# Kernel optimization log

Hardware: AMD Instinct MI355X
Metric: run time of the kernel (lower is better)

Reference implementation:

```python
import jax, jax.numpy as jnp
import numpy as np

B, S, H = 1, 2048, 1024
NH, NKV, HD = 16, 4, 64
I, E, K = 2816, 8, 2
WIN = 512
EPS = 1e-5


def setup_inputs() -> dict:
    key = jax.random.key(0)
    ks = jax.random.split(key, 8)
    sd = 0.02
    return {
        "hidden_states": jax.random.normal(ks[0], (B, S, H), jnp.float32),
        "positions": jnp.arange(S, dtype=jnp.int64),
        "w_qkv": jax.random.normal(ks[1], ((NH + 2 * NKV) * HD, H), jnp.float32) * sd,
        "w_o": jax.random.normal(ks[2], (H, NH * HD), jnp.float32) * sd,
        "router_w": jax.random.normal(ks[3], (E, H), jnp.float32) * sd,
        "ws": jax.random.normal(ks[4], (E, 2 * I, H), jnp.float32) * sd,
        "w2s": jax.random.normal(ks[5], (E, H, I), jnp.float32) * sd,
        "ln1_w": jnp.ones((H,), jnp.float32),
        "ln2_w": jnp.ones((H,), jnp.float32),
    }


def _rmsnorm(x, w):
    return x * jax.lax.rsqrt(jnp.mean(x * x, axis=-1, keepdims=True) + EPS) * w


def reference(hidden_states, positions, w_qkv, w_o, router_w, ws, w2s, ln1_w, ln2_w):
    # residual is None on entry -> residual = input, then input_layernorm
    residual = hidden_states
    x = _rmsnorm(hidden_states, ln1_w)

    # qkv projection (torch Linear: y = x @ W.T), GQA split
    qkv = jnp.einsum("bsh,oh->bso", x, w_qkv)
    q_size, kv_size = NH * HD, NKV * HD
    q = qkv[..., :q_size].reshape(B, S, NH, HD)
    k = qkv[..., q_size:q_size + kv_size].reshape(B, S, NKV, HD)
    v = qkv[..., q_size + kv_size:].reshape(B, S, NKV, HD)
    rep = NH // NKV
    k = jnp.repeat(k, rep, axis=2)  # [B,S,NH,HD]
    v = jnp.repeat(v, rep, axis=2)

    scale = HD ** -0.5
    scores = jnp.einsum("bqhd,bkhd->bhqk", q, k) * scale
    i = jnp.arange(S)[:, None]
    j = jnp.arange(S)[None, :]
    mask = (j <= i) & ((i - j) < WIN)  # causal sliding window
    scores = jnp.where(mask, scores, jnp.finfo(scores.dtype).min)
    attn = jax.nn.softmax(scores, axis=-1)
    o = jnp.einsum("bhqk,bkhd->bqhd", attn, v).reshape(B, S, NH * HD)
    attn_out = jnp.einsum("bso,ho->bsh", o, w_o)

    # pre_moe_layernorm with residual: x += residual; residual = x; x = norm(x)
    x2 = attn_out + residual
    residual2 = x2
    h = _rmsnorm(x2, ln2_w)

    # MoE: router softmax, top-k (renormalize=False), per-expert SwiGLU FFN
    t = h.reshape(-1, H)  # [T,H]
    logits = jnp.einsum("th,eh->te", t, router_w)
    probs = jax.nn.softmax(logits, axis=-1)
    vals, idx = jax.lax.top_k(probs, K)  # [T,K]
    w_dense = jnp.sum(vals[:, :, None] * jax.nn.one_hot(idx, E, dtype=t.dtype), axis=1)  # [T,E]

    out = jnp.zeros_like(t)
    for e in range(E):
        gu = jnp.einsum("th,ih->ti", t, ws[e])  # [T,2I]
        g, u = gu[:, :I], gu[:, I:]
        a = jax.nn.silu(g) * u
        y = jnp.einsum("ti,hi->th", a, w2s[e])
        out = out + w_dense[:, e:e + 1] * y

    return out.reshape(B, S, H), residual2
```

## Files before the change

### kernel.cpp

```cpp
#include <hip/hip_runtime.h>
#include <stdint.h>

typedef unsigned short u16;
typedef __attribute__((ext_vector_type(8))) short short8;
typedef __attribute__((ext_vector_type(4))) float f32x4;

constexpr int SEQ   = 2048;
constexpr int HID   = 1024;
constexpr int NHEAD = 16;
constexpr int QKVD  = 1536;
constexpr int FFI   = 2816;
constexpr int NEXP  = 8;
constexpr int WINSZ = 512;
#define EPSF 1e-5f

__device__ __forceinline__ u16 f2bf(float f) {
  union { unsigned int i; float f; } v; v.f = f;
  unsigned int i = v.i;
  return (u16)((i + 0x7fffu + ((i >> 16) & 1u)) >> 16);
}

__device__ __forceinline__ ushort4 f2bf4(float4 v) {
  ushort4 o;
  o.x = f2bf(v.x); o.y = f2bf(v.y); o.z = f2bf(v.z); o.w = f2bf(v.w);
  return o;
}

__device__ __forceinline__ void gload_lds16(const void* g, void* l) {
  __builtin_amdgcn_global_load_lds((__attribute__((address_space(1))) void*)g,
                                   (__attribute__((address_space(3))) void*)l,
                                   16, 0, 0);
}

#define MFMA_BF16(a, b, c) __builtin_amdgcn_mfma_f32_16x16x32_bf16(a, b, c, 0, 0, 0)

#define TILE_FENCE                                          \
  asm volatile("s_waitcnt vmcnt(0)" ::: "memory");          \
  __builtin_amdgcn_s_barrier();                             \
  __builtin_amdgcn_sched_barrier(0);

constexpr int CN3 = NEXP * 2 * FFI * HID / 4;
constexpr int CN4 = NEXP * HID * FFI / 4;
constexpr int CN_BIG   = CN3 + CN4;
constexpr int NCONV_BLK = CN_BIG / 1024;
constexpr int NATTN_BLK = (SEQ / 64) * NHEAD;

__global__ __launch_bounds__(256) void k_prep(const float* __restrict__ x,
                                              const float* __restrict__ w,
                                              u16* __restrict__ y) {
  const int bid = blockIdx.x, tid = threadIdx.x;
  const int wid = tid >> 6, lane = tid & 63;
  __shared__ float red[4];
  const float* xr = x + (size_t)bid * HID;
  float4 v = *(const float4*)&xr[tid * 4];
  float ss = v.x * v.x + v.y * v.y + v.z * v.z + v.w * v.w;
#pragma unroll
  for (int m = 1; m < 64; m <<= 1) ss += __shfl_xor(ss, m);
  if (lane == 0) red[wid] = ss;
  __syncthreads();
  ss = red[0] + red[1] + red[2] + red[3];
  float sc = rsqrtf(ss * (1.0f / HID) + EPSF);
  float4 wv = *(const float4*)&w[tid * 4];
  ushort4 o;
  o.x = f2bf(v.x * sc * wv.x);
  o.y = f2bf(v.y * sc * wv.y);
  o.z = f2bf(v.z * sc * wv.z);
  o.w = f2bf(v.w * sc * wv.w);
  *(ushort4*)&y[(size_t)bid * HID + tid * 4] = o;
}

__global__ __launch_bounds__(256, 2) void k_gemm_bt(
    const u16* __restrict__ A, const float* __restrict__ B,
    void* __restrict__ Cout, int N, int K, int KT, int wf32) {
  __shared__ u16 As[128 * 64];
  __shared__ u16 Bs[64 * 72];
  const int tid = threadIdx.x, wid = tid >> 6, lane = tid & 63;
  const int quad = lane >> 4, l16 = lane & 15;
  const int wr = wid >> 1, wc = wid & 1;
  const int m0 = blockIdx.y * 128, n0 = blockIdx.x * 64;
  const int M = gridDim.y * 128;
  const int kbase = blockIdx.z * KT * 64;
  const int sr = lane >> 3, sc = (lane & 7) * 8;
  const int brow = wid * 16 + (lane >> 2);
  const int bk = (lane & 3) * 16;
  f32x4 acc[4][2] = {};
  for (int kt = 0; kt < KT; ++kt) {
    const int k0 = kbase + (kt << 6);
    const float* bp = &B[(size_t)(n0 + brow) * K + k0 + bk];
    float4 bv0 = *(const float4*)&bp[0];
    float4 bv1 = *(const float4*)&bp[4];
    float4 bv2 = *(const float4*)&bp[8];
    float4 bv3 = *(const float4*)&bp[12];
#pragma unroll
    for (int it = 0; it < 4; ++it) {
      int seg = wid * 4 + it;
      int row = seg * 8 + sr;
      gload_lds16(&A[(size_t)(m0 + row) * K + k0 + sc], &As[seg * 512]);
    }
    *(ushort4*)&Bs[brow * 72 + bk + 0]  = f2bf4(bv0);
    *(ushort4*)&Bs[brow * 72 + bk + 4]  = f2bf4(bv1);
    *(ushort4*)&Bs[brow * 72 + bk + 8]  = f2bf4(bv2);
    *(ushort4*)&Bs[brow * 72 + bk + 12] = f2bf4(bv3);
    __syncthreads();
#pragma unroll
    for (int ks = 0; ks < 2; ++ks) {
      short8 af[4], bf[2];
#pragma unroll
      for (int t = 0; t < 4; ++t)
        af[t] = *(const short8*)&As[(64 * wr + 16 * t + l16) * 64 + ks * 32 + quad * 8];
#pragma unroll
      for (int t = 0; t < 2; ++t)
        bf[t] = *(const short8*)&Bs[(32 * wc + 16 * t + l16) * 72 + ks * 32 + quad * 8];
#pragma unroll
      for (int mt = 0; mt < 4; ++mt)
#pragma unroll
        for (int nt = 0; nt < 2; ++nt)
          acc[mt][nt] = MFMA_BF16(af[mt], bf[nt], acc[mt][nt]);
    }
    __syncthreads();
  }
  if (wf32) {
    float* C = (float*)Cout + (size_t)blockIdx.z * M * N;
#pragma unroll
    for (int mt = 0; mt < 4; ++mt)
#pragma unroll
      for (int r = 0; r < 4; ++r) {
        int row = m0 + 64 * wr + 16 * mt + quad * 4 + r;
#pragma unroll
        for (int nt = 0; nt < 2; ++nt) {
          int col = n0 + 32 * wc + 16 * nt + l16;
          C[(size_t)row * N + col] = acc[mt][nt][r];
        }
      }
  } else {
    u16* C = (u16*)Cout;
#pragma unroll
    for (int mt = 0; mt < 4; ++mt)
#pragma unroll
      for (int r = 0; r < 4; ++r) {
        int row = m0 + 64 * wr + 16 * mt + quad * 4 + r;
#pragma unroll
        for (int nt = 0; nt < 2; ++nt) {
          int col = n0 + 32 * wc + 16 * nt + l16;
          C[(size_t)row * N + col] = f2bf(acc[mt][nt][r]);
        }
      }
  }
}

__global__ __launch_bounds__(256, 2) void k_attn_conv(
    const u16* __restrict__ qkv, u16* __restrict__ o,
    const float* __restrict__ ws, const float* __restrict__ w2s,
    u16* __restrict__ dws, u16* __restrict__ dw2) {
  const int bid = blockIdx.x;
  const int tid = threadIdx.x;
  if (bid >= NATTN_BLK) {
    int j = (bid - NATTN_BLK) * 1024 + tid;
#pragma unroll
    for (int t = 0; t < 4; ++t) {
      int i = j + t * 256;
      const float* s; u16* d;
      if (i < CN3) { s = ws; d = dws; } else { i -= CN3; s = w2s; d = dw2; }
      float4 v = ((const float4*)s)[i];
      ushort4 u;
      u.x = f2bf(v.x); u.y = f2bf(v.y); u.z = f2bf(v.z); u.w = f2bf(v.w);
      ((ushort4*)d)[i] = u;
    }
    return;
  }
  const int qb = bid & 31;
  const int h  = bid >> 5;
  const int q0 = qb * 64;
  const int g = h >> 2;
  __shared__ u16 Qs[64 * 72], Ks[64 * 72], Vt[64 * 72], Ps[64 * 72];
  const int wid = tid >> 6, lane = tid & 63;
  const int quad = lane >> 4, l16 = lane & 15;

#pragma unroll
  for (int it = 0; it < 2; ++it) {
    int idx = it * 256 + tid;
    int row = idx >> 3, c8 = (idx & 7) * 8;
    *(short8*)&Qs[row * 72 + c8] =
        *(const short8*)&qkv[(size_t)(q0 + row) * QKVD + h * 64 + c8];
  }

  f32x4 oacc[4] = {};
  float mrun[4], lrun[4];
#pragma unroll
  for (int r = 0; r < 4; ++r) { mrun[r] = -1e30f; lrun[r] = 0.f; }

  const int ktlo = (q0 >= WINSZ) ? ((q0 - WINSZ + 1) >> 6) : 0;
  const int kthi = qb;
  for (int kt = ktlo; kt <= kthi; ++kt) {
#pragma unroll
    for (int it = 0; it < 2; ++it) {
      int idx = it * 256 + tid;
      int row = idx >> 3, c8 = (idx & 7) * 8;
      *(short8*)&Ks[row * 72 + c8] =
          *(const short8*)&qkv[(size_t)(kt * 64 + row) * QKVD + 1024 + g * 64 + c8];
    }
#pragma unroll
    for (int it = 0; it < 8; ++it) {
      int idx = it * 256 + tid;
      int key = idx >> 5;
      int d = (idx & 31) * 2;
      unsigned int u = *(const unsigned int*)&qkv[(size_t)(kt * 64 + key) * QKVD + 1280 + g * 64 + d];
      Vt[d * 72 + key] = (u16)(u & 0xffffu);
      Vt[(d + 1) * 72 + key] = (u16)(u >> 16);
    }
    __syncthreads();

    f32x4 sa[4] = {};
#pragma unroll
    for (int ks = 0; ks < 2; ++ks) {
      short8 af = *(const short8*)&Qs[(16 * wid + l16) * 72 + ks * 32 + quad * 8];
#pragma unroll
      for (int ct = 0; ct < 4; ++ct) {
        short8 bf = *(const short8*)&Ks[(16 * ct + l16) * 72 + ks * 32 + quad * 8];
        sa[ct] = MFMA_BF16(af, bf, sa[ct]);
      }
    }

    float pvv[4][4];
#pragma unroll
    for (int r = 0; r < 4; ++r) {
      int i = q0 + 16 * wid + quad * 4 + r;
      float mx = -1e30f;
#pragma unroll
      for (int ct = 0; ct < 4; ++ct) {
        int j = kt * 64 + 16 * ct + l16;
        float v = sa[ct][r] * 0.125f;
        bool ok = (j <= i) && (i - j < WINSZ);
        v = ok ? v : -1e30f;
        pvv[ct][r] = v;
        mx = fmaxf(mx, v);
      }
#pragma unroll
      for (int m = 1; m < 16; m <<= 1) mx = fmaxf(mx, __shfl_xor(mx, m));
      float mnew = fmaxf(mrun[r], mx);
      float alpha = __expf(mrun[r] - mnew);
      float s = 0.f;
#pragma unroll
      for (int ct = 0; ct < 4; ++ct) {
        float p = (pvv[ct][r] > -1e29f) ? __expf(pvv[ct][r] - mnew) : 0.f;
        pvv[ct][r] = p;
        s += p;
      }
#pragma unroll
      for (int m = 1; m < 16; m <<= 1) s += __shfl_xor(s, m);
      lrun[r] = lrun[r] * alpha + s;
      mrun[r] = mnew;
#pragma unroll
      for (int ct = 0; ct < 4; ++ct) oacc[ct][r] *= alpha;
    }
#pragma unroll
    for (int ct = 0; ct < 4; ++ct)
#pragma unroll
      for (int r = 0; r < 4; ++r)
        Ps[(16 * wid + quad * 4 + r) * 72 + 16 * ct + l16] = f2bf(pvv[ct][r]);
    __syncthreads();

#pragma unroll
    for (int ks = 0; ks < 2; ++ks) {
      short8 af = *(const short8*)&Ps[(16 * wid + l16) * 72 + ks * 32 + quad * 8];
#pragma unroll
      for (int ct = 0; ct < 4; ++ct) {
        short8 bf = *(const short8*)&Vt[(16 * ct + l16) * 72 + ks * 32 + quad * 8];
        oacc[ct] = MFMA_BF16(af, bf, oacc[ct]);
      }
    }
    __syncthreads();
  }

#pragma unroll
  for (int ct = 0; ct < 4; ++ct)
#pragma unroll
    for (int r = 0; r < 4; ++r) {
      int row = q0 + 16 * wid + quad * 4 + r;
      float v = oacc[ct][r] / lrun[r];
      o[(size_t)row * HID + h * 64 + 16 * ct + l16] = f2bf(v);
    }
}

__global__ __launch_bounds__(256) void k_rms2_router(
    const float* __restrict__ o0, const float* __restrict__ o1,
    const float* __restrict__ hs, const float* __restrict__ ln2,
    const float* __restrict__ rw, float* __restrict__ out1,
    u16* __restrict__ T, int* __restrict__ counts,
    int* __restrict__ tok_idx, int* __restrict__ tok_slot,
    float* __restrict__ tok_pw) {
  const int tkn = blockIdx.x, tid = threadIdx.x, wid = tid >> 6, lane = tid & 63;
  const size_t base = (size_t)tkn * HID + tid * 4;
  float4 a = *(const float4*)&o0[base];
  float4 b = *(const float4*)&o1[base];
  float4 h = *(const float4*)&hs[base];
  float4 v;
  v.x = a.x + b.x + h.x; v.y = a.y + b.y + h.y;
  v.z = a.z + b.z + h.z; v.w = a.w + b.w + h.w;
  *(float4*)&out1[base] = v;
  float ss = v.x * v.x + v.y * v.y + v.z * v.z + v.w * v.w;
#pragma unroll
  for (int m = 1; m < 64; m <<= 1) ss += __shfl_xor(ss, m);
  __shared__ float red[4];
  if (lane == 0) red[wid] = ss;
  __syncthreads();
  ss = red[0] + red[1] + red[2] + red[3];
  float sc = rsqrtf(ss * (1.0f / HID) + EPSF);
  float4 lw = *(const float4*)&ln2[tid * 4];
  float t0 = v.x * sc * lw.x;
  float t1 = v.y * sc * lw.y;
  float t2 = v.z * sc * lw.z;
  float t3 = v.w * sc * lw.w;
  ushort4 o;
  o.x = f2bf(t0); o.y = f2bf(t1); o.z = f2bf(t2); o.w = f2bf(t3);
  *(ushort4*)&T[(size_t)tkn * HID + tid * 4] = o;

  float p[8];
#pragma unroll
  for (int e = 0; e < 8; ++e) {
    float4 r = *(const float4*)&rw[e * HID + tid * 4];
    p[e] = t0 * r.x + t1 * r.y + t2 * r.z + t3 * r.w;
  }
#pragma unroll
  for (int e = 0; e < 8; ++e)
#pragma unroll
    for (int m = 1; m < 64; m <<= 1) p[e] += __shfl_xor(p[e], m);
  __shared__ float pr[4][8];
  if (lane == 0)
#pragma unroll
    for (int e = 0; e < 8; ++e) pr[wid][e] = p[e];
  __syncthreads();
  if (tid == 0) {
    float lg[8];
#pragma unroll
    for (int e = 0; e < 8; ++e) lg[e] = pr[0][e] + pr[1][e] + pr[2][e] + pr[3][e];
    float mx = lg[0];
#pragma unroll
    for (int e = 1; e < 8; ++e) mx = fmaxf(mx, lg[e]);
    float ex[8], se = 0.f;
#pragma unroll
    for (int e = 0; e < 8; ++e) { ex[e] = __expf(lg[e] - mx); se += ex[e]; }
    int b0 = 0;
#pragma unroll
    for (int e = 1; e < 8; ++e) if (lg[e] > lg[b0]) b0 = e;
    int b1 = (b0 == 0) ? 1 : 0;
#pragma unroll
    for (int e = 0; e < 8; ++e) if (e != b0 && lg[e] > lg[b1]) b1 = e;
    float inv = 1.0f / se;
    int s0 = atomicAdd(&counts[b0], 1);
    tok_idx[b0 * SEQ + s0] = tkn;
    tok_slot[2 * tkn] = b0 * SEQ + s0;
    tok_pw[2 * tkn] = ex[b0] * inv;
    int s1 = atomicAdd(&counts[b1], 1);
    tok_idx[b1 * SEQ + s1] = tkn;
    tok_slot[2 * tkn + 1] = b1 * SEQ + s1;
    tok_pw[2 * tkn + 1] = ex[b1] * inv;
  }
}

__global__ void k_offsets(const int* __restrict__ counts, int* __restrict__ offs) {
  if (threadIdx.x == 0 && blockIdx.x == 0) {
    int s = 0;
    for (int e = 0; e < NEXP; ++e) { offs[e] = s; s += counts[e]; }
    offs[NEXP] = s;
  }
}

__global__ __launch_bounds__(512, 2) void k_moe_gu(
    const u16* __restrict__ T, const u16* __restrict__ Wgu,
    const int* __restrict__ counts, const int* __restrict__ offs,
    const int* __restrict__ tok_idx, u16* __restrict__ Abuf) {
  const int e = blockIdx.z;
  const int cnt = counts[e];
  const int m0 = blockIdx.y * 256;
  if (m0 >= cnt) return;
  const int n0 = blockIdx.x * 128;
  const u16* We = Wgu + (size_t)e * 2 * FFI * HID;
  const int* ti = tok_idx + e * SEQ;
  const int aoff = offs[e];
  __shared__ u16 As[2][256 * 64], Bg[2][128 * 64], Bu[2][128 * 64];
  const int tid = threadIdx.x, wid = tid >> 6, lane = tid & 63;
  const int quad = lane >> 4, l16 = lane & 15;
  const int wr = wid >> 2, wc = wid & 3;
  const int sr = lane >> 3, sc = (lane & 7) * 8;
  int tokrow[4];
#pragma unroll
  for (int it = 0; it < 4; ++it) {
    int row = (wid * 4 + it) * 8 + sr;
    int ra = m0 + row;
    if (ra > cnt - 1) ra = cnt - 1;
    tokrow[it] = ti[ra];
  }
  f32x4 accg[8][2] = {}, accu[8][2] = {};

#define MSTAGE(buf, k0)                                                              \
  {                                                                                  \
    _Pragma("unroll") for (int it = 0; it < 4; ++it) {                               \
      int seg = wid * 4 + it;                                                        \
      gload_lds16(&T[(size_t)tokrow[it] * HID + (k0) + sc], &As[buf][seg * 512]);    \
    }                                                                                \
    _Pragma("unroll") for (int it = 0; it < 2; ++it) {                               \
      int seg = wid * 2 + it;                                                        \
      int row = seg * 8 + sr;                                                        \
      gload_lds16(&We[(size_t)(n0 + row) * HID + (k0) + sc], &Bg[buf][seg * 512]);   \
      gload_lds16(&We[(size_t)(FFI + n0 + row) * HID + (k0) + sc],                   \
                  &Bu[buf][seg * 512]);                                              \
    }                                                                                \
  }
#define MCOMP(buf)                                                                   \
  {                                                                                  \
    _Pragma("unroll") for (int ks = 0; ks < 2; ++ks) {                               \
      short8 af[8], bg[2], bu[2];                                                    \
      _Pragma("unroll") for (int t = 0; t < 8; ++t)                                  \
        af[t] = *(const short8*)&As[buf][(128 * wr + 16 * t + l16) * 64 + ks * 32 +  \
                                         quad * 8];                                  \
      _Pragma("unroll") for (int t = 0; t < 2; ++t) {                                \
        bg[t] = *(const short8*)&Bg[buf][(32 * wc + 16 * t + l16) * 64 + ks * 32 +   \
                                         quad * 8];                                  \
        bu[t] = *(const short8*)&Bu[buf][(32 * wc + 16 * t + l16) * 64 + ks * 32 +   \
                                         quad * 8];                                  \
      }                                                                              \
      _Pragma("unroll") for (int mt = 0; mt < 8; ++mt)                               \
        _Pragma("unroll") for (int nt = 0; nt < 2; ++nt) {                           \
          accg[mt][nt] = MFMA_BF16(af[mt], bg[nt], accg[mt][nt]);                    \
          accu[mt][nt] = MFMA_BF16(af[mt], bu[nt], accu[mt][nt]);                    \
        }                                                                            \
    }                                                                                \
  }

  MSTAGE(0, 0);
  TILE_FENCE
  int cur = 0;
  for (int kt = 0; kt < 16; ++kt) {
    if (kt + 1 < 16) MSTAGE(cur ^ 1, (kt + 1) << 6);
    MCOMP(cur);
    if (kt + 1 < 16) { TILE_FENCE }
    cur ^= 1;
  }
#undef MSTAGE
#undef MCOMP
#pragma unroll
  for (int mt = 0; mt < 8; ++mt)
#pragma unroll
    for (int r = 0; r < 4; ++r) {
      int rl = 128 * wr + 16 * mt + quad * 4 + r;
      int grow = m0 + rl;
      if (grow < cnt) {
        size_t rbase = (size_t)(aoff + grow) * FFI;
#pragma unroll
        for (int nt = 0; nt < 2; ++nt) {
          int col = n0 + 32 * wc + 16 * nt + l16;
          float gv = accg[mt][nt][r];
          float uv = accu[mt][nt][r];
          float a = gv / (1.0f + __expf(-gv)) * uv;
          Abuf[rbase + col] = f2bf(a);
        }
      }
    }
}

__global__ __launch_bounds__(512, 2) void k_moe_y(
    const u16* __restrict__ Abuf, const u16* __restrict__ W2,
    const int* __restrict__ counts, const int* __restrict__ offs,
    float* __restrict__ ybuf) {
  const int e = blockIdx.z >> 1;
  const int sk = blockIdx.z & 1;
  const int cnt = counts[e];
  const int m0 = blockIdx.y * 128;
  if (m0 >= cnt) return;
  const int n0 = blockIdx.x * 256;
  const int kbase = sk * 1408;
  const u16* We = W2 + (size_t)e * HID * FFI;
  const int aoff = offs[e];
  __shared__ u16 As[2][128 * 64], Bs[2][256 * 64];
  const int tid = threadIdx.x, wid = tid >> 6, lane = tid & 63;
  const int quad = lane >> 4, l16 = lane & 15;
  const int wr = wid >> 2, wc = wid & 3;
  const int sr = lane >> 3, sc = (lane & 7) * 8;
  int arow[2];
#pragma unroll
  for (int it = 0; it < 2; ++it) {
    int row = (wid * 2 + it) * 8 + sr;
    int ra = m0 + row;
    if (ra > cnt - 1) ra = cnt - 1;
    arow[it] = aoff + ra;
  }
  f32x4 acc[4][4] = {};

#define YSTAGE(buf, k0)                                                              \
  {                                                                                  \
    _Pragma("unroll") for (int it = 0; it < 2; ++it) {                               \
      int seg = wid * 2 + it;                                                        \
      gload_lds16(&Abuf[(size_t)arow[it] * FFI + (k0) + sc], &As[buf][seg * 512]);   \
    }                                                                                \
    _Pragma("unroll") for (int it = 0; it < 4; ++it) {                               \
      int seg = wid * 4 + it;                                                        \
      int row = seg * 8 + sr;                                                        \
      gload_lds16(&We[(size_t)(n0 + row) * FFI + (k0) + sc], &Bs[buf][seg * 512]);   \
    }                                                                                \
  }
#define YCOMP(buf)                                                                   \
  {                                                                                  \
    _Pragma("unroll") for (int ks = 0; ks < 2; ++ks) {                               \
      short8 af[4], bf[4];                                                           \
      _Pragma("unroll") for (int t = 0; t < 4; ++t)                                  \
        af[t] = *(const short8*)&As[buf][(64 * wr + 16 * t + l16) * 64 + ks * 32 +   \
                                         quad * 8];                                  \
      _Pragma("unroll") for (int t = 0; t < 4; ++t)                                  \
        bf[t] = *(const short8*)&Bs[buf][(64 * wc + 16 * t + l16) * 64 + ks * 32 +   \
                                         quad * 8];                                  \
      _Pragma("unroll") for (int mt = 0; mt < 4; ++mt)                               \
        _Pragma("unroll") for (int nt = 0; nt < 4; ++nt)                             \
            acc[mt][nt] = MFMA_BF16(af[mt], bf[nt], acc[mt][nt]);                    \
    }                                                                                \
  }

  YSTAGE(0, kbase);
  TILE_FENCE
  int cur = 0;
  for (int kt = 0; kt < 22; ++kt) {
    if (kt + 1 < 22) YSTAGE(cur ^ 1, kbase + ((kt + 1) << 6));
    YCOMP(cur);
    if (kt + 1 < 22) { TILE_FENCE }
    cur ^= 1;
  }
#undef YSTAGE
#undef YCOMP
  float* Y = ybuf + (size_t)sk * 2 * SEQ * HID;
#pragma unroll
  for (int mt = 0; mt < 4; ++mt)
#pragma unroll
    for (int r = 0; r < 4; ++r) {
      int rl = 64 * wr + 16 * mt + quad * 4 + r;
      int grow = m0 + rl;
      if (grow < cnt) {
        size_t obase = (size_t)(aoff + grow) * HID;
#pragma unroll
        for (int nt = 0; nt < 4; ++nt) {
          int col = n0 + 64 * wc + 16 * nt + l16;
          Y[obase + col] = acc[mt][nt][r];
        }
      }
    }
}

__global__ __launch_bounds__(256) void k_moe_out(
    const float* __restrict__ yb, const int* __restrict__ offs,
    const int* __restrict__ tok_slot, const float* __restrict__ tok_pw,
    float* __restrict__ out0) {
  const int t = blockIdx.x, tid = threadIdx.x;
  const int v0 = tok_slot[2 * t], v1 = tok_slot[2 * t + 1];
  const float w0 = tok_pw[2 * t], w1 = tok_pw[2 * t + 1];
  const size_t g0 = (size_t)(offs[v0 >> 11] + (v0 & (SEQ - 1))) * HID;
  const size_t g1 = (size_t)(offs[v1 >> 11] + (v1 & (SEQ - 1))) * HID;
  const size_t YP = (size_t)2 * SEQ * HID;
  const int c = tid * 4;
  float4 a0 = *(const float4*)&yb[g0 + c];
  float4 b0 = *(const float4*)&yb[YP + g0 + c];
  float4 a1 = *(const float4*)&yb[g1 + c];
  float4 b1 = *(const float4*)&yb[YP + g1 + c];
  float4 r;
  r.x = w0 * (a0.x + b0.x) + w1 * (a1.x + b1.x);
  r.y = w0 * (a0.y + b0.y) + w1 * (a1.y + b1.y);
  r.z = w0 * (a0.z + b0.z) + w1 * (a1.z + b1.z);
  r.w = w0 * (a0.w + b0.w) + w1 * (a1.w + b1.w);
  *(float4*)&out0[(size_t)t * HID + c] = r;
}

extern "C" void kernel_launch(void* const* d_in, const int* in_sizes, int n_in,
                              void* d_out, int out_size, void* d_ws, size_t ws_size,
                              hipStream_t stream) {
  const float* hs   = (const float*)d_in[0];
  const float* wqkv = (const float*)d_in[2];
  const float* wo   = (const float*)d_in[3];
  const float* rwt  = (const float*)d_in[4];
  const float* wsx  = (const float*)d_in[5];
  const float* w2s  = (const float*)d_in[6];
  const float* ln1  = (const float*)d_in[7];
  const float* ln2  = (const float*)d_in[8];
  float* out0 = (float*)d_out;
  float* out1 = out0 + (size_t)SEQ * HID;

  char* p = (char*)d_ws;
  u16* xn       = (u16*)p;   p += (size_t)SEQ * HID * 2;
  u16* qkv      = (u16*)p;   p += (size_t)SEQ * QKVD * 2;
  u16* ob       = (u16*)p;   p += (size_t)SEQ * HID * 2;
  float* of     = (float*)p; p += (size_t)2 * SEQ * HID * 4;
  int* counts   = (int*)p;   p += 32;
  int* offs     = (int*)p;   p += 64;
  int* tok_idx  = (int*)p;   p += (size_t)NEXP * SEQ * 4;
  int* tok_slot = (int*)p;   p += (size_t)2 * SEQ * 4;
  float* tok_pw = (float*)p; p += (size_t)2 * SEQ * 4;
  u16* abuf     = (u16*)p;   p += (size_t)2 * SEQ * FFI * 2;
  float* ybuf   = (float*)p; p += (size_t)2 * 2 * SEQ * HID * 4;
  u16* ws_b     = (u16*)p;   p += (size_t)NEXP * 2 * FFI * HID * 2;
  u16* w2s_b    = (u16*)p;   p += (size_t)NEXP * HID * FFI * 2;

  u16* tb = xn;

  hipMemsetAsync(counts, 0, 32, stream);

  k_prep<<<SEQ, 256, 0, stream>>>(hs, ln1, xn);
  k_gemm_bt<<<dim3(QKVD / 64, SEQ / 128, 1), 256, 0, stream>>>(
      xn, wqkv, qkv, QKVD, HID, 16, 0);
  k_attn_conv<<<NATTN_BLK + NCONV_BLK, 256, 0, stream>>>(
      qkv, ob, wsx, w2s, ws_b, w2s_b);
  k_gemm_bt<<<dim3(HID / 64, SEQ / 128, 2), 256, 0, stream>>>(
      ob, wo, of, HID, HID, 8, 1);
  k_rms2_router<<<SEQ, 256, 0, stream>>>(of, of + (size_t)SEQ * HID, hs, ln2,
                                         rwt, out1, tb, counts, tok_idx,
                                         tok_slot, tok_pw);
  k_offsets<<<1, 64, 0, stream>>>(counts, offs);
  k_moe_gu<<<dim3(FFI / 128, SEQ / 256, NEXP), 512, 0, stream>>>(
      tb, ws_b, counts, offs, tok_idx, abuf);
  k_moe_y<<<dim3(HID / 256, SEQ / 128, NEXP * 2), 512, 0, stream>>>(
      abuf, w2s_b, counts, offs, ybuf);
  k_moe_out<<<SEQ, 256, 0, stream>>>(ybuf, offs, tok_slot, tok_pw, out0);
}
```

Before: 678.0 us.

## XOR-swizzle LDS tiles and keep two global loads in flight in MoE GEMMs

Applies an XOR swizzle to the 16-byte column chunks of LDS tiles in the dense GEMM and both MoE expert GEMMs, so the MFMA fragment reads avoid LDS bank conflicts. The MoE gate/up and down kernels also replace the wait-all fence with partial vmcnt waits. This keeps the next tile's direct-to-LDS loads in flight while the current tile is computed, with stage k+2 issued only after a barrier marks the buffer free. The cost is more index arithmetic, and correctness now depends on the vmcnt counts matching the number of loads issued per stage.

Measured after the change: 637.3 us. 6.0% less time.

```diff
diff --git a/kernel.cpp b/kernel.cpp
--- a/kernel.cpp
+++ b/kernel.cpp
@@ -34,10 +34,8 @@
 
 #define MFMA_BF16(a, b, c) __builtin_amdgcn_mfma_f32_16x16x32_bf16(a, b, c, 0, 0, 0)
 
-#define TILE_FENCE                                          \
-  asm volatile("s_waitcnt vmcnt(0)" ::: "memory");          \
-  __builtin_amdgcn_s_barrier();                             \
-  __builtin_amdgcn_sched_barrier(0);
+#define SBAR  __builtin_amdgcn_s_barrier()
+#define SCHB  __builtin_amdgcn_sched_barrier(0)
 
 constexpr int CN3 = NEXP * 2 * FFI * HID / 4;
 constexpr int CN4 = NEXP * HID * FFI / 4;
@@ -80,7 +78,9 @@
   const int m0 = blockIdx.y * 128, n0 = blockIdx.x * 64;
   const int M = gridDim.y * 128;
   const int kbase = blockIdx.z * KT * 64;
-  const int sr = lane >> 3, sc = (lane & 7) * 8;
+  const int sr = lane >> 3;
+  const int scs = (((lane & 7) ^ sr) * 8);
+  const int rx = l16 & 7;
   const int brow = wid * 16 + (lane >> 2);
   const int bk = (lane & 3) * 16;
   f32x4 acc[4][2] = {};
@@ -95,7 +95,7 @@
     for (int it = 0; it < 4; ++it) {
       int seg = wid * 4 + it;
       int row = seg * 8 + sr;
-      gload_lds16(&A[(size_t)(m0 + row) * K + k0 + sc], &As[seg * 512]);
+      gload_lds16(&A[(size_t)(m0 + row) * K + k0 + scs], &As[seg * 512]);
     }
     *(ushort4*)&Bs[brow * 72 + bk + 0]  = f2bf4(bv0);
     *(ushort4*)&Bs[brow * 72 + bk + 4]  = f2bf4(bv1);
@@ -104,10 +104,11 @@
     __syncthreads();
 #pragma unroll
     for (int ks = 0; ks < 2; ++ks) {
+      const int cof = ((((ks << 2) | quad) ^ rx) << 3);
       short8 af[4], bf[2];
 #pragma unroll
       for (int t = 0; t < 4; ++t)
-        af[t] = *(const short8*)&As[(64 * wr + 16 * t + l16) * 64 + ks * 32 + quad * 8];
+        af[t] = *(const short8*)&As[(64 * wr + 16 * t + l16) * 64 + cof];
 #pragma unroll
       for (int t = 0; t < 2; ++t)
         bf[t] = *(const short8*)&Bs[(32 * wc + 16 * t + l16) * 72 + ks * 32 + quad * 8];
@@ -382,7 +383,9 @@
   const int tid = threadIdx.x, wid = tid >> 6, lane = tid & 63;
   const int quad = lane >> 4, l16 = lane & 15;
   const int wr = wid >> 2, wc = wid & 3;
-  const int sr = lane >> 3, sc = (lane & 7) * 8;
+  const int sr = lane >> 3;
+  const int scs = (((lane & 7) ^ sr) * 8);
+  const int rx = l16 & 7;
   int tokrow[4];
 #pragma unroll
   for (int it = 0; it < 4; ++it) {
@@ -397,28 +400,26 @@
   {                                                                                  \
     _Pragma("unroll") for (int it = 0; it < 4; ++it) {                               \
       int seg = wid * 4 + it;                                                        \
-      gload_lds16(&T[(size_t)tokrow[it] * HID + (k0) + sc], &As[buf][seg * 512]);    \
+      gload_lds16(&T[(size_t)tokrow[it] * HID + (k0) + scs], &As[buf][seg * 512]);   \
     }                                                                                \
     _Pragma("unroll") for (int it = 0; it < 2; ++it) {                               \
       int seg = wid * 2 + it;                                                        \
       int row = seg * 8 + sr;                                                        \
-      gload_lds16(&We[(size_t)(n0 + row) * HID + (k0) + sc], &Bg[buf][seg * 512]);   \
-      gload_lds16(&We[(size_t)(FFI + n0 + row) * HID + (k0) + sc],                   \
+      gload_lds16(&We[(size_t)(n0 + row) * HID + (k0) + scs], &Bg[buf][seg * 512]);  \
+      gload_lds16(&We[(size_t)(FFI + n0 + row) * HID + (k0) + scs],                  \
                   &Bu[buf][seg * 512]);                                              \
     }                                                                                \
   }
 #define MCOMP(buf)                                                                   \
   {                                                                                  \
     _Pragma("unroll") for (int ks = 0; ks < 2; ++ks) {                               \
+      const int cof = ((((ks << 2) | quad) ^ rx) << 3);                              \
       short8 af[8], bg[2], bu[2];                                                    \
       _Pragma("unroll") for (int t = 0; t < 8; ++t)                                  \
-        af[t] = *(const short8*)&As[buf][(128 * wr + 16 * t + l16) * 64 + ks * 32 +  \
-                                         quad * 8];                                  \
+        af[t] = *(const short8*)&As[buf][(128 * wr + 16 * t + l16) * 64 + cof];      \
       _Pragma("unroll") for (int t = 0; t < 2; ++t) {                                \
-        bg[t] = *(const short8*)&Bg[buf][(32 * wc + 16 * t + l16) * 64 + ks * 32 +   \
-                                         quad * 8];                                  \
-        bu[t] = *(const short8*)&Bu[buf][(32 * wc + 16 * t + l16) * 64 + ks * 32 +   \
-                                         quad * 8];                                  \
+        bg[t] = *(const short8*)&Bg[buf][(32 * wc + 16 * t + l16) * 64 + cof];       \
+        bu[t] = *(const short8*)&Bu[buf][(32 * wc + 16 * t + l16) * 64 + cof];       \
       }                                                                              \
       _Pragma("unroll") for (int mt = 0; mt < 8; ++mt)                               \
         _Pragma("unroll") for (int nt = 0; nt < 2; ++nt) {                           \
@@ -429,13 +430,17 @@
   }
 
   MSTAGE(0, 0);
-  TILE_FENCE
-  int cur = 0;
+  MSTAGE(1, 64);
   for (int kt = 0; kt < 16; ++kt) {
-    if (kt + 1 < 16) MSTAGE(cur ^ 1, (kt + 1) << 6);
-    MCOMP(cur);
-    if (kt + 1 < 16) { TILE_FENCE }
-    cur ^= 1;
+    if (kt < 15) {
+      asm volatile("s_waitcnt vmcnt(8)" ::: "memory");
+    } else {
+      asm volatile("s_waitcnt vmcnt(0)" ::: "memory");
+    }
+    SBAR; SCHB;
+    MCOMP(kt & 1);
+    SCHB; SBAR;
+    if (kt + 2 < 16) MSTAGE(kt & 1, (kt + 2) << 6);
   }
 #undef MSTAGE
 #undef MCOMP
@@ -476,7 +481,9 @@
   const int tid = threadIdx.x, wid = tid >> 6, lane = tid & 63;
   const int quad = lane >> 4, l16 = lane & 15;
   const int wr = wid >> 2, wc = wid & 3;
-  const int sr = lane >> 3, sc = (lane & 7) * 8;
+  const int sr = lane >> 3;
+  const int scs = (((lane & 7) ^ sr) * 8);
+  const int rx = l16 & 7;
   int arow[2];
 #pragma unroll
   for (int it = 0; it < 2; ++it) {
@@ -491,24 +498,23 @@
   {                                                                                  \
     _Pragma("unroll") for (int it = 0; it < 2; ++it) {                               \
       int seg = wid * 2 + it;                                                        \
-      gload_lds16(&Abuf[(size_t)arow[it] * FFI + (k0) + sc], &As[buf][seg * 512]);   \
+      gload_lds16(&Abuf[(size_t)arow[it] * FFI + (k0) + scs], &As[buf][seg * 512]);  \
     }                                                                                \
     _Pragma("unroll") for (int it = 0; it < 4; ++it) {                               \
       int seg = wid * 4 + it;                                                        \
       int row = seg * 8 + sr;                                                        \
-      gload_lds16(&We[(size_t)(n0 + row) * FFI + (k0) + sc], &Bs[buf][seg * 512]);   \
+      gload_lds16(&We[(size_t)(n0 + row) * FFI + (k0) + scs], &Bs[buf][seg * 512]);  \
     }                                                                                \
   }
 #define YCOMP(buf)                                                                   \
   {                                                                                  \
     _Pragma("unroll") for (int ks = 0; ks < 2; ++ks) {                               \
+      const int cof = ((((ks << 2) | quad) ^ rx) << 3);                              \
       short8 af[4], bf[4];                                                           \
       _Pragma("unroll") for (int t = 0; t < 4; ++t)                                  \
-        af[t] = *(const short8*)&As[buf][(64 * wr + 16 * t + l16) * 64 + ks * 32 +   \
-                                         quad * 8];                                  \
+        af[t] = *(const short8*)&As[buf][(64 * wr + 16 * t + l16) * 64 + cof];       \
       _Pragma("unroll") for (int t = 0; t < 4; ++t)                                  \
-        bf[t] = *(const short8*)&Bs[buf][(64 * wc + 16 * t + l16) * 64 + ks * 32 +   \
-                                         quad * 8];                                  \
+        bf[t] = *(const short8*)&Bs[buf][(64 * wc + 16 * t + l16) * 64 + cof];       \
       _Pragma("unroll") for (int mt = 0; mt < 4; ++mt)                               \
         _Pragma("unroll") for (int nt = 0; nt < 4; ++nt)                             \
             acc[mt][nt] = MFMA_BF16(af[mt], bf[nt], acc[mt][nt]);                    \
@@ -516,13 +522,17 @@
   }
 
   YSTAGE(0, kbase);
-  TILE_FENCE
-  int cur = 0;
+  YSTAGE(1, kbase + 64);
   for (int kt = 0; kt < 22; ++kt) {
-    if (kt + 1 < 22) YSTAGE(cur ^ 1, kbase + ((kt + 1) << 6));
-    YCOMP(cur);
-    if (kt + 1 < 22) { TILE_FENCE }
-    cur ^= 1;
+    if (kt < 21) {
+      asm volatile("s_waitcnt vmcnt(6)" ::: "memory");
+    } else {
+      asm volatile("s_waitcnt vmcnt(0)" ::: "memory");
+    }
+    SBAR; SCHB;
+    YCOMP(kt & 1);
+    SCHB; SBAR;
+    if (kt + 2 < 22) YSTAGE(kt & 1, kbase + ((kt + 2) << 6));
   }
 #undef YSTAGE
 #undef YCOMP
```
